# Kernel tuning notes

Hardware: AMD Instinct MI355X
Metric: run time of the kernel (lower is better)

Reference implementation:

```python
import jax, jax.numpy as jnp
import numpy as np

N = 100000
E = 1600000
D_IN = 128
HID = 128
OUT = 64


def _sage_conv(x, edge_index, W_l, W_r, b, num_nodes):
    # PyG SAGEConv (aggr='mean'): out = lin_l(mean_{j in N(i)} x_j) + lin_r(x_i)
    src, dst = edge_index[0], edge_index[1]
    msgs = x[src]  # [E, d] gather from source nodes
    summed = jax.ops.segment_sum(msgs, dst, num_segments=num_nodes)  # [N, d]
    cnt = jax.ops.segment_sum(jnp.ones((msgs.shape[0],), x.dtype), dst, num_segments=num_nodes)
    agg = summed / jnp.maximum(cnt, 1.0)[:, None]  # mean; isolated nodes -> 0
    return agg @ W_l + b + x @ W_r


def setup_inputs() -> dict:
    key = jax.random.key(0)
    ks = jax.random.split(key, 8)
    x = jax.random.normal(ks[0], (N, D_IN), dtype=jnp.float32)
    edge_index = jax.random.randint(ks[1], (2, E), 0, N, dtype=jnp.int64)
    s1 = 1.0 / np.sqrt(D_IN)
    s2 = 1.0 / np.sqrt(HID)
    W_l1 = jax.random.uniform(ks[2], (D_IN, HID), jnp.float32, -s1, s1)
    W_r1 = jax.random.uniform(ks[3], (D_IN, HID), jnp.float32, -s1, s1)
    b1 = jnp.zeros((HID,), jnp.float32)
    W_l2 = jax.random.uniform(ks[4], (HID, OUT), jnp.float32, -s2, s2)
    W_r2 = jax.random.uniform(ks[5], (HID, OUT), jnp.float32, -s2, s2)
    b2 = jnp.zeros((OUT,), jnp.float32)
    return {"x": x, "edge_index": edge_index, "W_l1": W_l1, "W_r1": W_r1,
            "b1": b1, "W_l2": W_l2, "W_r2": W_r2, "b2": b2}


def reference(x, edge_index, W_l1, W_r1, b1, W_l2, W_r2, b2):
    h = _sage_conv(x, edge_index, W_l1, W_r1, b1, N)
    h = jax.nn.relu(h)
    out = _sage_conv(h, edge_index, W_l2, W_r2, b2, N)
    return out
```

## Files before the change

kernel.cpp:

```cpp
#include <hip/hip_runtime.h>
#include <hip/hip_fp16.h>

typedef __attribute__((ext_vector_type(8))) short bf16x8;
typedef __attribute__((ext_vector_type(4))) float f32x4;

__device__ __forceinline__ f32x4 mfma16(bf16x8 a, bf16x8 b, f32x4 c) {
    return __builtin_amdgcn_mfma_f32_16x16x32_bf16(a, b, c, 0, 0, 0);
}

__device__ __forceinline__ unsigned short bf16_rte(float f) {
    unsigned int u = __float_as_uint(f);
    unsigned int r = (u + 0x7FFFu + ((u >> 16) & 1u)) >> 16;
    return (unsigned short)r;
}
__device__ __forceinline__ float bf16_f(unsigned short h) {
    return __uint_as_float(((unsigned int)h) << 16);
}

__device__ __forceinline__ void split8h(bf16x8 raw, bf16x8& hi, bf16x8& lo) {
#pragma unroll
    for (int j = 0; j < 8; ++j) {
        float f = __half2float(__ushort_as_half((unsigned short)raw[j]));
        unsigned short h = bf16_rte(f);
        hi[j] = (short)h;
        lo[j] = (short)bf16_rte(f - bf16_f(h));
    }
}

__global__ void k_wconv(const float* __restrict__ W, unsigned short* __restrict__ hi,
                        unsigned short* __restrict__ lo, int K, int F) {
    int e = blockIdx.x * 256 + threadIdx.x;
    if (e >= K * F) return;
    int col = e / K, k = e - col * K;
    float v = W[(size_t)k * F + col];
    unsigned short h = bf16_rte(v);
    hi[e] = h;
    lo[e] = bf16_rte(v - bf16_f(h));
}

__global__ __launch_bounds__(256) void k_xconv(const float* __restrict__ x,
                                               unsigned short* __restrict__ x16,
                                               int total8) {
    int i = blockIdx.x * 256 + threadIdx.x;
    if (i >= total8) return;
    const float4* xp = (const float4*)x + (size_t)i * 2;
    float4 a = xp[0], b = xp[1];
    bf16x8 o;
    o[0] = (short)__half_as_ushort(__float2half_rn(a.x));
    o[1] = (short)__half_as_ushort(__float2half_rn(a.y));
    o[2] = (short)__half_as_ushort(__float2half_rn(a.z));
    o[3] = (short)__half_as_ushort(__float2half_rn(a.w));
    o[4] = (short)__half_as_ushort(__float2half_rn(b.x));
    o[5] = (short)__half_as_ushort(__float2half_rn(b.y));
    o[6] = (short)__half_as_ushort(__float2half_rn(b.z));
    o[7] = (short)__half_as_ushort(__float2half_rn(b.w));
    *(bf16x8*)&x16[(size_t)i * 8] = o;
}


#define MAXNB 1024

__global__ __launch_bounds__(256) void k_bcount(
    const int* __restrict__ dst, int* __restrict__ bcnt, int E, int chunk, int nb) {
    __shared__ int h[MAXNB];
    int t = threadIdx.x;
    for (int i = t; i < nb; i += 256) h[i] = 0;
    __syncthreads();
    int base = blockIdx.x * chunk;
    int end = min(base + chunk, E);
    for (int i = base + t; i < end; i += 256) atomicAdd(&h[dst[i] >> 7], 1);
    __syncthreads();
    for (int i = t; i < nb; i += 256)
        if (h[i]) atomicAdd(&bcnt[i], h[i]);
}

__global__ void k_bscan(const int* __restrict__ bcnt, int* __restrict__ boff,
                        int* __restrict__ bcur, int nb) {
    __shared__ int sh[1024];
    int t = threadIdx.x;
    int v = (t < nb) ? bcnt[t] : 0;
    sh[t] = v;
    __syncthreads();
    for (int off = 1; off < 1024; off <<= 1) {
        int u = (t >= off) ? sh[t - off] : 0;
        __syncthreads();
        sh[t] += u;
        __syncthreads();
    }
    if (t < nb) {
        int ex = sh[t] - v;
        boff[t] = ex;
        bcur[t] = ex;
    }
}

__global__ __launch_bounds__(256) void k_bscatter(
    const int* __restrict__ src, const int* __restrict__ dst,
    int* __restrict__ bcur, int2* __restrict__ pairs, int E, int chunk, int nb) {
    __shared__ int h[MAXNB];
    __shared__ int curs[MAXNB];
    int t = threadIdx.x;
    for (int i = t; i < nb; i += 256) h[i] = 0;
    __syncthreads();
    int base = blockIdx.x * chunk;
    int end = min(base + chunk, E);
    for (int i = base + t; i < end; i += 256) atomicAdd(&h[dst[i] >> 7], 1);
    __syncthreads();
    for (int i = t; i < nb; i += 256)
        curs[i] = h[i] ? atomicAdd(&bcur[i], h[i]) : 0;
    __syncthreads();
    for (int i = base + t; i < end; i += 256) {
        int d = dst[i];
        int p = atomicAdd(&curs[d >> 7], 1);
        pairs[p] = make_int2(d, src[i]);
    }
}

__global__ __launch_bounds__(256) void k_build(
    const int2* __restrict__ pairs, const int* __restrict__ boff,
    int* __restrict__ csr, int* __restrict__ start, int* __restrict__ deg,
    int n, int nb, int E) {
    __shared__ int scnt[128];
    __shared__ int soff[128];
    __shared__ int cur[128];
    int b = blockIdx.x;
    int t = threadIdx.x;
    int base = boff[b];
    int end = (b + 1 < nb) ? boff[b + 1] : E;
    if (t < 128) scnt[t] = 0;
    __syncthreads();
    for (int i = base + t; i < end; i += 256) {
        int2 e = pairs[i];
        atomicAdd(&scnt[e.x & 127], 1);
    }
    __syncthreads();
    if (t < 128) soff[t] = scnt[t];
    __syncthreads();
    for (int off = 1; off < 128; off <<= 1) {
        int val = 0;
        if (t < 128 && t >= off) val = soff[t - off];
        __syncthreads();
        if (t < 128) soff[t] += val;
        __syncthreads();
    }
    if (t < 128) {
        int c = scnt[t];
        int ex = soff[t] - c;
        int node = b * 128 + t;
        if (node < n) {
            start[node] = base + ex;
            deg[node] = c;
        }
        cur[t] = base + ex;
    }
    __syncthreads();
    for (int i = base + t; i < end; i += 256) {
        int2 e = pairs[i];
        int p = atomicAdd(&cur[e.x & 127], 1);
        csr[p] = e.y;
    }
}


#define SR 40

template <int FOUT, bool S0F32, bool OUT_H16>
__device__ __forceinline__ void gemm_dual_body(
    const float* __restrict__ X0f, const unsigned short* __restrict__ X0h,
    const unsigned short* __restrict__ X1h,
    const unsigned short* __restrict__ W0H, const unsigned short* __restrict__ W0L,
    const unsigned short* __restrict__ W1H, const unsigned short* __restrict__ W1L,
    const float* __restrict__ bias, unsigned short* __restrict__ dstH,
    float* __restrict__ dstF, int n) {
    constexpr int CT = FOUT / 64;
    __shared__ unsigned short aHi[4][64 * SR], aLo[4][64 * SR];

    int t = threadIdx.x;
    int wv = t >> 6, l = t & 63, q = l >> 4, nl = l & 15;
    int wc = wv * (FOUT / 4);
    int node0 = blockIdx.x * 64;
    int sn = t >> 2, q4 = t & 3;
    int gn = min(node0 + sn, n - 1);

    bf16x8 s1r[4];
    {
        const unsigned short* p = X1h + (size_t)gn * 128 + q4 * 8;
#pragma unroll
        for (int c = 0; c < 4; ++c) s1r[c] = *(const bf16x8*)(p + c * 32);
    }
    bf16x8 w1h0[CT], w1l0[CT];
#pragma unroll
    for (int uu = 0; uu < CT; ++uu) {
        int base = (wc + uu * 16 + nl) * 128 + q * 8;
        w1h0[uu] = *(const bf16x8*)&W1H[base];
        w1l0[uu] = *(const bf16x8*)&W1L[base];
    }

    if (S0F32) {
        const float4* ap = (const float4*)(X0f + (size_t)gn * 128);
        float4 xa[8];
#pragma unroll
        for (int c = 0; c < 4; ++c) {
            xa[c * 2]     = ap[c * 8 + q4 * 2];
            xa[c * 2 + 1] = ap[c * 8 + q4 * 2 + 1];
        }
        int base = sn * SR + q4 * 8;
#pragma unroll
        for (int c = 0; c < 4; ++c) {
            ushort4 hi, lo;
            float4 v = xa[c * 2];
            hi.x = bf16_rte(v.x); lo.x = bf16_rte(v.x - bf16_f(hi.x));
            hi.y = bf16_rte(v.y); lo.y = bf16_rte(v.y - bf16_f(hi.y));
            hi.z = bf16_rte(v.z); lo.z = bf16_rte(v.z - bf16_f(hi.z));
            hi.w = bf16_rte(v.w); lo.w = bf16_rte(v.w - bf16_f(hi.w));
            *(ushort4*)&aHi[c][base] = hi;
            *(ushort4*)&aLo[c][base] = lo;
            v = xa[c * 2 + 1];
            hi.x = bf16_rte(v.x); lo.x = bf16_rte(v.x - bf16_f(hi.x));
            hi.y = bf16_rte(v.y); lo.y = bf16_rte(v.y - bf16_f(hi.y));
            hi.z = bf16_rte(v.z); lo.z = bf16_rte(v.z - bf16_f(hi.z));
            hi.w = bf16_rte(v.w); lo.w = bf16_rte(v.w - bf16_f(hi.w));
            *(ushort4*)&aHi[c][base + 4] = hi;
            *(ushort4*)&aLo[c][base + 4] = lo;
        }
    } else {
        const unsigned short* p = X0h + (size_t)gn * 128 + q4 * 8;
        bf16x8 r[4];
#pragma unroll
        for (int c = 0; c < 4; ++c) r[c] = *(const bf16x8*)(p + c * 32);
        int base = sn * SR + q4 * 8;
#pragma unroll
        for (int c = 0; c < 4; ++c) {
            bf16x8 hi, lo;
            split8h(r[c], hi, lo);
            *(bf16x8*)&aHi[c][base] = hi;
            *(bf16x8*)&aLo[c][base] = lo;
        }
    }

    f32x4 acc[4][CT];
#pragma unroll
    for (int a = 0; a < 4; ++a)
#pragma unroll
        for (int b = 0; b < CT; ++b) acc[a][b] = (f32x4){0.f, 0.f, 0.f, 0.f};

    bf16x8 wh[2][CT], wl[2][CT];
#pragma unroll
    for (int uu = 0; uu < CT; ++uu) {
        int base = (wc + uu * 16 + nl) * 128 + q * 8;
        wh[0][uu] = *(const bf16x8*)&W0H[base];
        wl[0][uu] = *(const bf16x8*)&W0L[base];
    }
    __syncthreads();

#pragma unroll
    for (int c = 0; c < 4; ++c) {
        if (c < 3) {
#pragma unroll
            for (int uu = 0; uu < CT; ++uu) {
                int base = (wc + uu * 16 + nl) * 128 + (c + 1) * 32 + q * 8;
                wh[(c + 1) & 1][uu] = *(const bf16x8*)&W0H[base];
                wl[(c + 1) & 1][uu] = *(const bf16x8*)&W0L[base];
            }
        }
        bf16x8 ah[4], al[4];
#pragma unroll
        for (int tt = 0; tt < 4; ++tt) {
            int off = (tt * 16 + nl) * SR + q * 8;
            ah[tt] = *(const bf16x8*)&aHi[c][off];
            al[tt] = *(const bf16x8*)&aLo[c][off];
        }
        int cb = c & 1;
#pragma unroll
        for (int tt = 0; tt < 4; ++tt)
#pragma unroll
            for (int uu = 0; uu < CT; ++uu) {
                f32x4 a = acc[tt][uu];
                a = mfma16(al[tt], wh[cb][uu], a);
                a = mfma16(ah[tt], wl[cb][uu], a);
                a = mfma16(ah[tt], wh[cb][uu], a);
                acc[tt][uu] = a;
            }
    }
    __syncthreads();

    {
        int base = sn * SR + q4 * 8;
#pragma unroll
        for (int c = 0; c < 4; ++c) {
            bf16x8 hi, lo;
            split8h(s1r[c], hi, lo);
            *(bf16x8*)&aHi[c][base] = hi;
            *(bf16x8*)&aLo[c][base] = lo;
        }
    }
#pragma unroll
    for (int uu = 0; uu < CT; ++uu) { wh[0][uu] = w1h0[uu]; wl[0][uu] = w1l0[uu]; }
    __syncthreads();

#pragma unroll
    for (int c = 0; c < 4; ++c) {
        if (c < 3) {
#pragma unroll
            for (int uu = 0; uu < CT; ++uu) {
                int base = (wc + uu * 16 + nl) * 128 + (c + 1) * 32 + q * 8;
                wh[(c + 1) & 1][uu] = *(const bf16x8*)&W1H[base];
                wl[(c + 1) & 1][uu] = *(const bf16x8*)&W1L[base];
            }
        }
        bf16x8 ah[4], al[4];
#pragma unroll
        for (int tt = 0; tt < 4; ++tt) {
            int off = (tt * 16 + nl) * SR + q * 8;
            ah[tt] = *(const bf16x8*)&aHi[c][off];
            al[tt] = *(const bf16x8*)&aLo[c][off];
        }
        int cb = c & 1;
#pragma unroll
        for (int tt = 0; tt < 4; ++tt)
#pragma unroll
            for (int uu = 0; uu < CT; ++uu) {
                f32x4 a = acc[tt][uu];
                a = mfma16(al[tt], wh[cb][uu], a);
                a = mfma16(ah[tt], wl[cb][uu], a);
                a = mfma16(ah[tt], wh[cb][uu], a);
                acc[tt][uu] = a;
            }
    }
    __syncthreads();

    if (OUT_H16) {
        unsigned short* tb = &aHi[0][0];
#pragma unroll
        for (int uu = 0; uu < CT; ++uu) {
            int col = wc + uu * 16 + nl;
            float bv = bias[col];
#pragma unroll
            for (int tt = 0; tt < 4; ++tt)
#pragma unroll
                for (int r = 0; r < 4; ++r) {
                    float vv = fmaxf(acc[tt][uu][r] + bv, 0.f);
                    tb[(tt * 16 + q * 4 + r) * 136 + col] =
                        __half_as_ushort(__float2half_rn(vv));
                }
        }
        __syncthreads();
        int node = node0 + sn;
        if (node < n) {
            const unsigned short* sp = tb + sn * 136 + q4 * 32;
            unsigned short* dp = dstH + (size_t)node * 128 + q4 * 32;
#pragma unroll
            for (int i = 0; i < 4; ++i) *(bf16x8*)(dp + i * 8) = *(const bf16x8*)(sp + i * 8);
        }
    } else {
        float* tb = (float*)&aHi[0][0];
#pragma unroll
        for (int uu = 0; uu < CT; ++uu) {
            int col = wc + uu * 16 + nl;
            float bv = bias[col];
#pragma unroll
            for (int tt = 0; tt < 4; ++tt)
#pragma unroll
                for (int r = 0; r < 4; ++r)
                    tb[(tt * 16 + q * 4 + r) * 68 + col] = acc[tt][uu][r] + bv;
        }
        __syncthreads();
        int node = node0 + sn;
        if (node < n) {
            const float* sp = tb + sn * 68 + q4 * 16;
            float* dp = dstF + (size_t)node * 64 + q4 * 16;
#pragma unroll
            for (int i = 0; i < 4; ++i) *(float4*)(dp + i * 4) = *(const float4*)(sp + i * 4);
        }
    }
}

__global__ __launch_bounds__(256, 2) void gemm1f(
    const float* __restrict__ X, const unsigned short* __restrict__ XM,
    const unsigned short* WrH, const unsigned short* WrL,
    const unsigned short* WlH, const unsigned short* WlL,
    const float* __restrict__ bias, unsigned short* __restrict__ h16, int n) {
    gemm_dual_body<128, true, true>(X, nullptr, XM, WrH, WrL, WlH, WlL, bias, h16, nullptr, n);
}

__global__ __launch_bounds__(256, 2) void gemm2f(
    const unsigned short* __restrict__ H, const unsigned short* __restrict__ HM,
    const unsigned short* WrH, const unsigned short* WrL,
    const unsigned short* WlH, const unsigned short* WlL,
    const float* __restrict__ bias, float* __restrict__ out, int n) {
    gemm_dual_body<64, false, false>(nullptr, H, HM, WrH, WrL, WlH, WlL, bias, nullptr, out, n);
}

__global__ void aggF(const unsigned short* __restrict__ tab, const int* __restrict__ csr,
                     const int* __restrict__ start, const int* __restrict__ deg,
                     unsigned short* __restrict__ outm, int n) {
    int gid = blockIdx.x * blockDim.x + threadIdx.x;
    int wave = gid >> 6, lane = gid & 63;
    int half = lane >> 5, fl = lane & 31;
    int node = wave * 2 + half;
    if (node >= n) return;
    int s = start[node], d = deg[node];
    const float2* u2 = (const float2*)tab;
    float4 A = {0.f, 0.f, 0.f, 0.f}, B = {0.f, 0.f, 0.f, 0.f};
    int j = 0;
    for (; j + 4 <= d; j += 4) {
        int i0 = csr[s + j], i1 = csr[s + j + 1], i2 = csr[s + j + 2], i3 = csr[s + j + 3];
        float2 r0 = u2[(size_t)i0 * 32 + fl];
        float2 r1 = u2[(size_t)i1 * 32 + fl];
        float2 r2 = u2[(size_t)i2 * 32 + fl];
        float2 r3 = u2[(size_t)i3 * 32 + fl];
        float2 a0 = __half22float2(*(const __half2*)&r0.x), b0 = __half22float2(*(const __half2*)&r0.y);
        float2 a1 = __half22float2(*(const __half2*)&r1.x), b1 = __half22float2(*(const __half2*)&r1.y);
        float2 a2 = __half22float2(*(const __half2*)&r2.x), b2 = __half22float2(*(const __half2*)&r2.y);
        float2 a3 = __half22float2(*(const __half2*)&r3.x), b3 = __half22float2(*(const __half2*)&r3.y);
        A.x += a0.x + a1.x; A.y += a0.y + a1.y;
        A.z += b0.x + b1.x; A.w += b0.y + b1.y;
        B.x += a2.x + a3.x; B.y += a2.y + a3.y;
        B.z += b2.x + b3.x; B.w += b2.y + b3.y;
    }
    for (; j < d; ++j) {
        float2 r0 = u2[(size_t)csr[s + j] * 32 + fl];
        float2 a0 = __half22float2(*(const __half2*)&r0.x), b0 = __half22float2(*(const __half2*)&r0.y);
        A.x += a0.x; A.y += a0.y; A.z += b0.x; A.w += b0.y;
    }
    float inv = 1.0f / (float)max(d, 1);
    float mx = (A.x + B.x) * inv, my = (A.y + B.y) * inv;
    float mz = (A.z + B.z) * inv, mw = (A.w + B.w) * inv;
    __half2 h01 = __floats2half2_rn(mx, my);
    __half2 h23 = __floats2half2_rn(mz, mw);
    uint2 w;
    w.x = *(unsigned int*)&h01;
    w.y = *(unsigned int*)&h23;
    *(uint2*)&outm[(size_t)node * 128 + fl * 4] = w;
}


extern "C" void kernel_launch(void* const* d_in, const int* in_sizes, int n_in,
                              void* d_out, int out_size, void* d_ws, size_t ws_size,
                              hipStream_t stream) {
    const float* x   = (const float*)d_in[0];
    const int*   ei  = (const int*)d_in[1];
    const float* Wl1 = (const float*)d_in[2];
    const float* Wr1 = (const float*)d_in[3];
    const float* b1  = (const float*)d_in[4];
    const float* Wl2 = (const float*)d_in[5];
    const float* Wr2 = (const float*)d_in[6];
    const float* b2  = (const float*)d_in[7];
    float* out = (float*)d_out;

    int Nn = in_sizes[0] / 128;
    int E  = in_sizes[1] / 2;
    const int* src = ei;
    const int* dst = ei + E;
    int nb = (Nn + 127) / 128;

    char* ws = (char*)d_ws;
    auto alloc = [&](size_t bytes) -> char* {
        char* pp = ws;
        ws += (bytes + 255) / 256 * 256;
        return pp;
    };
    int* bcnt   = (int*)alloc((size_t)nb * 4);
    int* boff   = (int*)alloc((size_t)nb * 4);
    int* bcur   = (int*)alloc((size_t)nb * 4);
    int* start  = (int*)alloc((size_t)Nn * 4);
    int* deg    = (int*)alloc((size_t)Nn * 4);
    int* csr    = (int*)alloc((size_t)E * 4);
    unsigned short* x16  = (unsigned short*)alloc((size_t)Nn * 128 * 2);
    unsigned short* xm16 = (unsigned short*)alloc((size_t)Nn * 128 * 2);
    unsigned short* h16  = (unsigned short*)alloc((size_t)Nn * 128 * 2);
    unsigned short* hm16 = (unsigned short*)alloc((size_t)Nn * 128 * 2);
    unsigned short* w1ah = (unsigned short*)alloc(128 * 128 * 2);
    unsigned short* w1al = (unsigned short*)alloc(128 * 128 * 2);
    unsigned short* w1bh = (unsigned short*)alloc(128 * 128 * 2);
    unsigned short* w1bl = (unsigned short*)alloc(128 * 128 * 2);
    unsigned short* w2ah = (unsigned short*)alloc(64 * 128 * 2);
    unsigned short* w2al = (unsigned short*)alloc(64 * 128 * 2);
    unsigned short* w2bh = (unsigned short*)alloc(64 * 128 * 2);
    unsigned short* w2bl = (unsigned short*)alloc(64 * 128 * 2);
    int2* pairs = (int2*)hm16;

    hipMemsetAsync(bcnt, 0, (size_t)nb * 4, stream);

    k_wconv<<<64, 256, 0, stream>>>(Wl1, w1ah, w1al, 128, 128);
    k_wconv<<<64, 256, 0, stream>>>(Wr1, w1bh, w1bl, 128, 128);
    k_wconv<<<32, 256, 0, stream>>>(Wl2, w2ah, w2al, 128, 64);
    k_wconv<<<32, 256, 0, stream>>>(Wr2, w2bh, w2bl, 128, 64);
    k_xconv<<<(Nn * 16 + 255) / 256, 256, 0, stream>>>(x, x16, Nn * 16);

    int chunk = (E + 255) / 256;
    k_bcount<<<256, 256, 0, stream>>>(dst, bcnt, E, chunk, nb);
    k_bscan<<<1, 1024, 0, stream>>>(bcnt, boff, bcur, nb);
    k_bscatter<<<256, 256, 0, stream>>>(src, dst, bcur, pairs, E, chunk, nb);
    k_build<<<nb, 256, 0, stream>>>(pairs, boff, csr, start, deg, Nn, nb, E);

    int gb = (Nn + 63) / 64;
    aggF<<<(Nn + 7) / 8, 256, 0, stream>>>(x16, csr, start, deg, xm16, Nn);
    gemm1f<<<gb, 256, 0, stream>>>(x, xm16, w1bh, w1bl, w1ah, w1al, b1, h16, Nn);
    aggF<<<(Nn + 7) / 8, 256, 0, stream>>>(h16, csr, start, deg, hm16, Nn);
    gemm2f<<<gb, 256, 0, stream>>>(h16, hm16, w2bh, w2bl, w2ah, w2al, b2, out, Nn);
}
```

Before: 377.4 us.

## Slice feature tables by column groups for cache-local neighbor aggregation

Stores the fp16 feature tables (input x and hidden h) in a column-sliced layout: eight slices of 16 features, each contiguous over all nodes. The new aggregation kernel works on one slice per block, so the gathered working set for random neighbors is a 3.2 MB slice that can stay in cache. Each wave now spreads a node's edges across 8 lane groups and reduces them with shuffles. The cost is an extra sliced copy of h written by the first GEMM and narrower 8-byte gathers per edge, with csr/start/deg read eight times.

```diff
diff --git a/kernel.cpp b/kernel.cpp
--- a/kernel.cpp
+++ b/kernel.cpp
@@ -38,23 +38,34 @@
     lo[e] = bf16_rte(v - bf16_f(h));
 }
 
-__global__ __launch_bounds__(256) void k_xconv(const float* __restrict__ x,
-                                               unsigned short* __restrict__ x16,
-                                               int total8) {
-    int i = blockIdx.x * 256 + threadIdx.x;
-    if (i >= total8) return;
-    const float4* xp = (const float4*)x + (size_t)i * 2;
-    float4 a = xp[0], b = xp[1];
-    bf16x8 o;
-    o[0] = (short)__half_as_ushort(__float2half_rn(a.x));
-    o[1] = (short)__half_as_ushort(__float2half_rn(a.y));
-    o[2] = (short)__half_as_ushort(__float2half_rn(a.z));
-    o[3] = (short)__half_as_ushort(__float2half_rn(a.w));
-    o[4] = (short)__half_as_ushort(__float2half_rn(b.x));
-    o[5] = (short)__half_as_ushort(__float2half_rn(b.y));
-    o[6] = (short)__half_as_ushort(__float2half_rn(b.z));
-    o[7] = (short)__half_as_ushort(__float2half_rn(b.w));
-    *(bf16x8*)&x16[(size_t)i * 8] = o;
+__global__ __launch_bounds__(256) void k_xslice(const float* __restrict__ x,
+                                                unsigned short* __restrict__ xs,
+                                                int n) {
+    int t = blockIdx.x * 256 + threadIdx.x;
+    int node = t >> 3, s = t & 7;
+    if (node >= n) return;
+    const float4* p = (const float4*)(x + (size_t)node * 128 + s * 16);
+    float4 v0 = p[0], v1 = p[1], v2 = p[2], v3 = p[3];
+    bf16x8 o0, o1;
+    o0[0] = (short)__half_as_ushort(__float2half_rn(v0.x));
+    o0[1] = (short)__half_as_ushort(__float2half_rn(v0.y));
+    o0[2] = (short)__half_as_ushort(__float2half_rn(v0.z));
+    o0[3] = (short)__half_as_ushort(__float2half_rn(v0.w));
+    o0[4] = (short)__half_as_ushort(__float2half_rn(v1.x));
+    o0[5] = (short)__half_as_ushort(__float2half_rn(v1.y));
+    o0[6] = (short)__half_as_ushort(__float2half_rn(v1.z));
+    o0[7] = (short)__half_as_ushort(__float2half_rn(v1.w));
+    o1[0] = (short)__half_as_ushort(__float2half_rn(v2.x));
+    o1[1] = (short)__half_as_ushort(__float2half_rn(v2.y));
+    o1[2] = (short)__half_as_ushort(__float2half_rn(v2.z));
+    o1[3] = (short)__half_as_ushort(__float2half_rn(v2.w));
+    o1[4] = (short)__half_as_ushort(__float2half_rn(v3.x));
+    o1[5] = (short)__half_as_ushort(__float2half_rn(v3.y));
+    o1[6] = (short)__half_as_ushort(__float2half_rn(v3.z));
+    o1[7] = (short)__half_as_ushort(__float2half_rn(v3.w));
+    unsigned short* dp = xs + ((size_t)s * n + node) * 16;
+    *(bf16x8*)dp = o0;
+    *(bf16x8*)(dp + 8) = o1;
 }
 
 
@@ -171,7 +182,7 @@
     const unsigned short* __restrict__ W0H, const unsigned short* __restrict__ W0L,
     const unsigned short* __restrict__ W1H, const unsigned short* __restrict__ W1L,
     const float* __restrict__ bias, unsigned short* __restrict__ dstH,
-    float* __restrict__ dstF, int n) {
+    unsigned short* __restrict__ dstS, float* __restrict__ dstF, int n) {
     constexpr int CT = FOUT / 64;
     __shared__ unsigned short aHi[4][64 * SR], aLo[4][64 * SR];
 
@@ -351,6 +362,12 @@
             unsigned short* dp = dstH + (size_t)node * 128 + q4 * 32;
 #pragma unroll
             for (int i = 0; i < 4; ++i) *(bf16x8*)(dp + i * 8) = *(const bf16x8*)(sp + i * 8);
+            unsigned short* e0 = dstS + ((size_t)(q4 * 2) * n + node) * 16;
+            unsigned short* e1 = dstS + ((size_t)(q4 * 2 + 1) * n + node) * 16;
+            *(bf16x8*)e0 = *(const bf16x8*)sp;
+            *(bf16x8*)(e0 + 8) = *(const bf16x8*)(sp + 8);
+            *(bf16x8*)e1 = *(const bf16x8*)(sp + 16);
+            *(bf16x8*)(e1 + 8) = *(const bf16x8*)(sp + 24);
         }
     } else {
         float* tb = (float*)&aHi[0][0];
@@ -379,8 +396,9 @@
     const float* __restrict__ X, const unsigned short* __restrict__ XM,
     const unsigned short* WrH, const unsigned short* WrL,
     const unsigned short* WlH, const unsigned short* WlL,
-    const float* __restrict__ bias, unsigned short* __restrict__ h16, int n) {
-    gemm_dual_body<128, true, true>(X, nullptr, XM, WrH, WrL, WlH, WlL, bias, h16, nullptr, n);
+    const float* __restrict__ bias, unsigned short* __restrict__ h16,
+    unsigned short* __restrict__ h16s, int n) {
+    gemm_dual_body<128, true, true>(X, nullptr, XM, WrH, WrL, WlH, WlL, bias, h16, h16s, nullptr, n);
 }
 
 __global__ __launch_bounds__(256, 2) void gemm2f(
@@ -388,50 +406,50 @@
     const unsigned short* WrH, const unsigned short* WrL,
     const unsigned short* WlH, const unsigned short* WlL,
     const float* __restrict__ bias, float* __restrict__ out, int n) {
-    gemm_dual_body<64, false, false>(nullptr, H, HM, WrH, WrL, WlH, WlL, bias, nullptr, out, n);
-}
-
-__global__ void aggF(const unsigned short* __restrict__ tab, const int* __restrict__ csr,
-                     const int* __restrict__ start, const int* __restrict__ deg,
-                     unsigned short* __restrict__ outm, int n) {
-    int gid = blockIdx.x * blockDim.x + threadIdx.x;
-    int wave = gid >> 6, lane = gid & 63;
-    int half = lane >> 5, fl = lane & 31;
-    int node = wave * 2 + half;
-    if (node >= n) return;
-    int s = start[node], d = deg[node];
-    const float2* u2 = (const float2*)tab;
-    float4 A = {0.f, 0.f, 0.f, 0.f}, B = {0.f, 0.f, 0.f, 0.f};
-    int j = 0;
-    for (; j + 4 <= d; j += 4) {
-        int i0 = csr[s + j], i1 = csr[s + j + 1], i2 = csr[s + j + 2], i3 = csr[s + j + 3];
-        float2 r0 = u2[(size_t)i0 * 32 + fl];
-        float2 r1 = u2[(size_t)i1 * 32 + fl];
-        float2 r2 = u2[(size_t)i2 * 32 + fl];
-        float2 r3 = u2[(size_t)i3 * 32 + fl];
-        float2 a0 = __half22float2(*(const __half2*)&r0.x), b0 = __half22float2(*(const __half2*)&r0.y);
-        float2 a1 = __half22float2(*(const __half2*)&r1.x), b1 = __half22float2(*(const __half2*)&r1.y);
-        float2 a2 = __half22float2(*(const __half2*)&r2.x), b2 = __half22float2(*(const __half2*)&r2.y);
-        float2 a3 = __half22float2(*(const __half2*)&r3.x), b3 = __half22float2(*(const __half2*)&r3.y);
-        A.x += a0.x + a1.x; A.y += a0.y + a1.y;
-        A.z += b0.x + b1.x; A.w += b0.y + b1.y;
-        B.x += a2.x + a3.x; B.y += a2.y + a3.y;
-        B.z += b2.x + b3.x; B.w += b2.y + b3.y;
-    }
-    for (; j < d; ++j) {
-        float2 r0 = u2[(size_t)csr[s + j] * 32 + fl];
-        float2 a0 = __half22float2(*(const __half2*)&r0.x), b0 = __half22float2(*(const __half2*)&r0.y);
-        A.x += a0.x; A.y += a0.y; A.z += b0.x; A.w += b0.y;
-    }
-    float inv = 1.0f / (float)max(d, 1);
-    float mx = (A.x + B.x) * inv, my = (A.y + B.y) * inv;
-    float mz = (A.z + B.z) * inv, mw = (A.w + B.w) * inv;
-    __half2 h01 = __floats2half2_rn(mx, my);
-    __half2 h23 = __floats2half2_rn(mz, mw);
-    uint2 w;
-    w.x = *(unsigned int*)&h01;
-    w.y = *(unsigned int*)&h23;
-    *(uint2*)&outm[(size_t)node * 128 + fl * 4] = w;
+    gemm_dual_body<64, false, false>(nullptr, H, HM, WrH, WrL, WlH, WlL, bias, nullptr, nullptr, out, n);
+}
+
+__global__ __launch_bounds__(256) void aggS(
+    const unsigned short* __restrict__ tabS, const int* __restrict__ csr,
+    const int* __restrict__ start, const int* __restrict__ deg,
+    unsigned short* __restrict__ outm, int n) {
+    int bid = blockIdx.x;
+    int s = bid & 7, chunk = bid >> 3;
+    int t = threadIdx.x;
+    int wv = t >> 6, l = t & 63;
+    int half = l >> 5, eg = (l >> 2) & 7, cq = l & 3;
+    const unsigned short* tab = tabS + (size_t)s * n * 16;
+    int nbase = chunk * 64 + wv * 16;
+#pragma unroll 1
+    for (int i = 0; i < 16; i += 2) {
+        int node = nbase + i + half;
+        if (node < n) {
+            int st = __builtin_nontemporal_load(&start[node]);
+            int d = __builtin_nontemporal_load(&deg[node]);
+            float a0 = 0.f, a1 = 0.f, a2 = 0.f, a3 = 0.f;
+            for (int j = eg; j < d; j += 8) {
+                int idx = __builtin_nontemporal_load(&csr[st + j]);
+                const __half2* p = (const __half2*)(tab + (size_t)idx * 16 + cq * 4);
+                float2 u0 = __half22float2(p[0]);
+                float2 u1 = __half22float2(p[1]);
+                a0 += u0.x; a1 += u0.y; a2 += u1.x; a3 += u1.y;
+            }
+            for (int off = 4; off <= 16; off <<= 1) {
+                a0 += __shfl_xor(a0, off);
+                a1 += __shfl_xor(a1, off);
+                a2 += __shfl_xor(a2, off);
+                a3 += __shfl_xor(a3, off);
+            }
+            if (eg == 0) {
+                float inv = 1.f / (float)max(d, 1);
+                __half2 h01 = __floats2half2_rn(a0 * inv, a1 * inv);
+                __half2 h23 = __floats2half2_rn(a2 * inv, a3 * inv);
+                unsigned int* wp = (unsigned int*)&outm[(size_t)node * 128 + s * 16 + cq * 4];
+                __builtin_nontemporal_store(*(unsigned int*)&h01, wp);
+                __builtin_nontemporal_store(*(unsigned int*)&h23, wp + 1);
+            }
+        }
+    }
 }
 
 
@@ -466,9 +484,10 @@
     int* start  = (int*)alloc((size_t)Nn * 4);
     int* deg    = (int*)alloc((size_t)Nn * 4);
     int* csr    = (int*)alloc((size_t)E * 4);
-    unsigned short* x16  = (unsigned short*)alloc((size_t)Nn * 128 * 2);
+    unsigned short* x16s = (unsigned short*)alloc((size_t)Nn * 128 * 2);
     unsigned short* xm16 = (unsigned short*)alloc((size_t)Nn * 128 * 2);
     unsigned short* h16  = (unsigned short*)alloc((size_t)Nn * 128 * 2);
+    unsigned short* h16s = (unsigned short*)alloc((size_t)Nn * 128 * 2);
     unsigned short* hm16 = (unsigned short*)alloc((size_t)Nn * 128 * 2);
     unsigned short* w1ah = (unsigned short*)alloc(128 * 128 * 2);
     unsigned short* w1al = (unsigned short*)alloc(128 * 128 * 2);
@@ -486,7 +505,7 @@
     k_wconv<<<64, 256, 0, stream>>>(Wr1, w1bh, w1bl, 128, 128);
     k_wconv<<<32, 256, 0, stream>>>(Wl2, w2ah, w2al, 128, 64);
     k_wconv<<<32, 256, 0, stream>>>(Wr2, w2bh, w2bl, 128, 64);
-    k_xconv<<<(Nn * 16 + 255) / 256, 256, 0, stream>>>(x, x16, Nn * 16);
+    k_xslice<<<(Nn * 8 + 255) / 256, 256, 0, stream>>>(x, x16s, Nn);
 
     int chunk = (E + 255) / 256;
     k_bcount<<<256, 256, 0, stream>>>(dst, bcnt, E, chunk, nb);
@@ -495,8 +514,9 @@
     k_build<<<nb, 256, 0, stream>>>(pairs, boff, csr, start, deg, Nn, nb, E);
 
     int gb = (Nn + 63) / 64;
-    aggF<<<(Nn + 7) / 8, 256, 0, stream>>>(x16, csr, start, deg, xm16, Nn);
-    gemm1f<<<gb, 256, 0, stream>>>(x, xm16, w1bh, w1bl, w1ah, w1al, b1, h16, Nn);
-    aggF<<<(Nn + 7) / 8, 256, 0, stream>>>(h16, csr, start, deg, hm16, Nn);
+    int ga = ((Nn + 63) / 64) * 8;
+    aggS<<<ga, 256, 0, stream>>>(x16s, csr, start, deg, xm16, Nn);
+    gemm1f<<<gb, 256, 0, stream>>>(x, xm16, w1bh, w1bl, w1ah, w1al, b1, h16, h16s, Nn);
+    aggS<<<ga, 256, 0, stream>>>(h16s, csr, start, deg, hm16, Nn);
     gemm2f<<<gb, 256, 0, stream>>>(h16, hm16, w2bh, w2bl, w2ah, w2al, b2, out, Nn);
 }
```

New measurement: 699.4 us. 85.3% more time.
